# Performance work log

Measured on AMD Instinct MI355X. Metric: run time of the kernel, lower is better.

The kernel has to match this reference:

```python
import jax, jax.numpy as jnp
import numpy as np

V, E, H, TAGS = 50000, 128, 128, 8  # H = hidden per direction (hidden_dim // 2)
B, T = 64, 512


def _lstm_dir(x, w_ih, w_hh, b_ih, b_hh, reverse):
    # x: [B,T,I] -> hs: [B,T,H]; PyTorch gate order i,f,g,o
    xg = jnp.einsum('bti,gi->btg', x, w_ih) + b_ih + b_hh  # [B,T,4H]
    if reverse:
        xg = xg[:, ::-1]
    Bn = x.shape[0]
    Hn = w_hh.shape[1]

    def step(carry, g):
        h, c = carry
        g = g + h @ w_hh.T
        i, f, gg, o = jnp.split(g, 4, axis=-1)
        c = jax.nn.sigmoid(f) * c + jax.nn.sigmoid(i) * jnp.tanh(gg)
        h = jax.nn.sigmoid(o) * jnp.tanh(c)
        return (h, c), h

    h0 = jnp.zeros((Bn, Hn), x.dtype)
    _, hs = jax.lax.scan(step, (h0, h0), jnp.swapaxes(xg, 0, 1))
    hs = jnp.swapaxes(hs, 0, 1)
    return hs[:, ::-1] if reverse else hs


def _crf_partition(emissions, transitions):
    # emissions: [B,T,K]; scan the forward algorithm over time
    fv0 = emissions[:, 0]  # [B,K]

    def step(fv, emit):
        fv = jax.nn.logsumexp(fv[:, :, None] + transitions[None] + emit[:, None, :], axis=1)
        return fv, None

    fv, _ = jax.lax.scan(step, fv0, jnp.swapaxes(emissions[:, 1:], 0, 1))
    return jax.nn.logsumexp(fv, axis=1)  # [B]


def _forward_nll(sentences, tags, embedding, lstm_params, h2t_w, h2t_b, transitions):
    x = embedding[sentences]  # [B,T,E]; dropout inactive (eval)
    for pf, pb in lstm_params:
        x = jnp.concatenate([_lstm_dir(x, *pf, False), _lstm_dir(x, *pb, True)], axis=-1)
    emissions = x @ h2t_w.T + h2t_b  # [B,T,K]
    # gold path score (mask = all ones)
    emit_score = jnp.take_along_axis(emissions, tags[:, :, None], axis=2)[..., 0].sum(axis=1)
    trans_score = transitions[tags[:, :-1], tags[:, 1:]].sum(axis=1)
    partition = _crf_partition(emissions, transitions)
    return -(emit_score + trans_score - partition).mean()


def setup_inputs() -> dict:
    key = jax.random.key(0)
    ks = jax.random.split(key, 40)
    sc = 0.05
    inp = {}
    inp['sentences'] = jax.random.randint(ks[0], (B, T), 0, V)
    inp['tags'] = jax.random.randint(ks[1], (B, T), 0, TAGS)
    emb = jax.random.normal(ks[2], (V, E), jnp.float32) * sc
    inp['embedding'] = emb.at[0].set(0.0)  # padding_idx=0
    idx = 3
    for l in range(2):
        in_dim = E if l == 0 else 2 * H
        for d in ('', '_rev'):
            inp[f'w_ih_l{l}{d}'] = jax.random.normal(ks[idx], (4 * H, in_dim), jnp.float32) * sc; idx += 1
            inp[f'w_hh_l{l}{d}'] = jax.random.normal(ks[idx], (4 * H, H), jnp.float32) * sc; idx += 1
            inp[f'b_ih_l{l}{d}'] = jax.random.normal(ks[idx], (4 * H,), jnp.float32) * sc; idx += 1
            inp[f'b_hh_l{l}{d}'] = jax.random.normal(ks[idx], (4 * H,), jnp.float32) * sc; idx += 1
    inp['h2t_w'] = jax.random.normal(ks[idx], (TAGS, 2 * H), jnp.float32) * sc; idx += 1
    inp['h2t_b'] = jax.random.normal(ks[idx], (TAGS,), jnp.float32) * sc; idx += 1
    trans = jax.random.normal(ks[idx], (TAGS, TAGS), jnp.float32)
    inp['transitions'] = trans.at[0, :].set(-10000.0).at[:, 0].set(-10000.0)
    return inp


def reference(sentences, tags, embedding,
              w_ih_l0, w_hh_l0, b_ih_l0, b_hh_l0,
              w_ih_l0_rev, w_hh_l0_rev, b_ih_l0_rev, b_hh_l0_rev,
              w_ih_l1, w_hh_l1, b_ih_l1, b_hh_l1,
              w_ih_l1_rev, w_hh_l1_rev, b_ih_l1_rev, b_hh_l1_rev,
              h2t_w, h2t_b, transitions):
    lstm_params = [
        ((w_ih_l0, w_hh_l0, b_ih_l0, b_hh_l0), (w_ih_l0_rev, w_hh_l0_rev, b_ih_l0_rev, b_hh_l0_rev)),
        ((w_ih_l1, w_hh_l1, b_ih_l1, b_hh_l1), (w_ih_l1_rev, w_hh_l1_rev, b_ih_l1_rev, b_hh_l1_rev)),
    ]
    return _forward_nll(sentences, tags, embedding, lstm_params, h2t_w, h2t_b, transitions)
```

## Files before the change

kernel.cpp:

```cpp
#include <hip/hip_runtime.h>
#include <cstdint>
#include <cstddef>

typedef __attribute__((ext_vector_type(8))) short bf16x8;
typedef __attribute__((ext_vector_type(8))) int   v8i;
typedef __attribute__((ext_vector_type(4))) float f32x4;

__device__ __forceinline__ unsigned short f2bf(float x) {
    union { float f; unsigned u; } v; v.f = x;
    unsigned r = (v.u + 0x7fffu + ((v.u >> 16) & 1u)) >> 16;
    return (unsigned short)r;
}
__device__ __forceinline__ unsigned short f2bf_trunc(float x) {
    union { float f; unsigned u; } v; v.f = x;
    return (unsigned short)(v.u >> 16);
}
__device__ __forceinline__ float bflo(unsigned u){ union{unsigned i;float f;}v; v.i = u << 16;        return v.f; }
__device__ __forceinline__ float bfhi(unsigned u){ union{unsigned i;float f;}v; v.i = u & 0xffff0000u; return v.f; }
__device__ __forceinline__ float frcp(float x){ return __builtin_amdgcn_rcpf(x); }
__device__ __forceinline__ float fsig(float x){ return frcp(1.f + __expf(-x)); }
__device__ __forceinline__ float ftanh(float x){ return 2.f * frcp(1.f + __expf(-2.f * x)) - 1.f; }

#define BARRIER_LGKM() asm volatile("s_waitcnt lgkmcnt(0)\n\ts_barrier" ::: "memory")

#define BB 64
#define TT 512
#define MM (BB*TT)
#define NG 1024

__device__ __forceinline__ int perm_orig(int g2) {
    return (g2 & 3) * 128 + (g2 >> 6) * 16 + ((g2 >> 4) & 3) * 4 + ((g2 >> 2) & 3);
}

__global__ void prep_kernel(
    const int* __restrict__ sentences, const float* __restrict__ emb,
    const float* __restrict__ w_ih_l0, const float* __restrict__ w_ih_l0r,
    const float* __restrict__ w_ih_l1, const float* __restrict__ w_ih_l1r,
    const float* __restrict__ w_hh_l0, const float* __restrict__ w_hh_l0r,
    const float* __restrict__ w_hh_l1, const float* __restrict__ w_hh_l1r,
    const float* __restrict__ b_ih_l0, const float* __restrict__ b_hh_l0,
    const float* __restrict__ b_ih_l0r, const float* __restrict__ b_hh_l0r,
    const float* __restrict__ b_ih_l1, const float* __restrict__ b_hh_l1,
    const float* __restrict__ b_ih_l1r, const float* __restrict__ b_hh_l1r,
    unsigned short* __restrict__ x0, unsigned short* __restrict__ W0c,
    unsigned short* __restrict__ W1c,
    int* __restrict__ Whh0q, int* __restrict__ Whh1q,
    float* __restrict__ bias0, float* __restrict__ bias1)
{
    int blk = blockIdx.x;
    if (blk < 4096) {
        int t4 = blk * 256 + threadIdx.x;
        int e4 = t4 * 4; int m = e4 >> 7; int k = e4 & 127;
        int tt = m >> 6, b = m & 63;
        int s = sentences[b * 512 + tt];
        float4 v = *(const float4*)(emb + (size_t)s * 128 + k);
        *(ushort4*)(x0 + (size_t)m * 128 + k) =
            make_ushort4(f2bf(v.x), f2bf(v.y), f2bf(v.z), f2bf(v.w));
    } else if (blk < 4224) {
        int t4 = (blk - 4096) * 256 + threadIdx.x;
        int e4 = t4 * 4; int n = e4 >> 7; int k = e4 & 127;
        int dir = n >> 9; int orig = perm_orig(n & 511);
        const float* src = dir ? w_ih_l0r : w_ih_l0;
        float4 v = *(const float4*)(src + (size_t)orig * 128 + k);
        *(ushort4*)(W0c + (size_t)n * 128 + k) =
            make_ushort4(f2bf(v.x), f2bf(v.y), f2bf(v.z), f2bf(v.w));
    } else if (blk < 4480) {
        int t4 = (blk - 4224) * 256 + threadIdx.x;
        int e4 = t4 * 4; int n = e4 >> 8; int k = e4 & 255;
        int dir = n >> 9; int orig = perm_orig(n & 511);
        const float* src = dir ? w_ih_l1r : w_ih_l1;
        float4 v = *(const float4*)(src + (size_t)orig * 256 + k);
        *(ushort4*)(W1c + (size_t)n * 256 + k) =
            make_ushort4(f2bf(v.x), f2bf(v.y), f2bf(v.z), f2bf(v.w));
    } else if (blk < 4736) {
        int lb = blk - 4480;
        int layer = lb >> 7;
        int t4 = (lb & 127) * 256 + threadIdx.x;
        int f  = t4 * 4;
        int j0   = f & 31;
        int lp   = (f >> 5) & 63;
        int quad = lp >> 4, r = lp & 15;
        int tb   = f >> 11;
        int tile = tb & 3, w = (tb >> 2) & 7, dir = tb >> 5;
        int g2 = w * 64 + tile * 16 + r;
        int orig = perm_orig(g2);
        const float* src = layer ? (dir ? w_hh_l1r : w_hh_l1)
                                 : (dir ? w_hh_l0r : w_hh_l0);
        int k = quad * 32 + j0;
        float4 v = *(const float4*)(src + (size_t)orig * 128 + k);
        int p = __builtin_amdgcn_cvt_pk_fp8_f32(v.x * 64.f, v.y * 64.f, 0, false);
        p = __builtin_amdgcn_cvt_pk_fp8_f32(v.z * 64.f, v.w * 64.f, p, true);
        (layer ? Whh1q : Whh0q)[f >> 2] = p;
    } else {
        int t = (blk - 4736) * 256 + threadIdx.x;
        int n = t & 1023;
        int dir = n >> 9; int orig = perm_orig(n & 511);
        if (t < 1024)
            bias0[n] = dir ? (b_ih_l0r[orig] + b_hh_l0r[orig]) : (b_ih_l0[orig] + b_hh_l0[orig]);
        else
            bias1[n] = dir ? (b_ih_l1r[orig] + b_hh_l1r[orig]) : (b_ih_l1[orig] + b_hh_l1[orig]);
    }
}

__global__ __launch_bounds__(256, 2) void gemm_xg(
    const unsigned short* __restrict__ W,
    const unsigned short* __restrict__ X,
    const float* __restrict__ bias,
    unsigned short* __restrict__ xgS,
    int K)
{
    __shared__ unsigned short sW[128 * 32];
    __shared__ unsigned short sX[128 * 32];
    const int tid  = threadIdx.x;
    const int lane = tid & 63;
    const int wid  = tid >> 6;
    const int w_n  = wid & 1, w_m = wid >> 1;
    const int r16  = lane & 15, quad = lane >> 4;
    const int nTile = blockIdx.x * 128;
    const int mTile = blockIdx.y * 128;

    f32x4 zero = {0.f, 0.f, 0.f, 0.f};
    f32x4 acc[4][4];
    #pragma unroll
    for (int i = 0; i < 4; ++i)
        #pragma unroll
        for (int j = 0; j < 4; ++j) acc[i][j] = zero;

    const int q0 = tid, q1 = tid + 256;
    const int r0 = q0 >> 2, c0 = q0 & 3, ko0 = c0 * 8;
    const int r1 = q1 >> 2, c1 = q1 & 3, ko1 = c1 * 8;
    const int s0 = (r0 << 2) | (c0 ^ ((r0 >> 1) & 3));
    const int s1 = (r1 << 2) | (c1 ^ ((r1 >> 1) & 3));
    const int rsw = quad ^ ((r16 >> 1) & 3);

    const unsigned short* Wp0 = W + (size_t)(nTile + r0) * K + ko0;
    const unsigned short* Wp1 = W + (size_t)(nTile + r1) * K + ko1;
    const unsigned short* Xp0 = X + (size_t)(mTile + r0) * K + ko0;
    const unsigned short* Xp1 = X + (size_t)(mTile + r1) * K + ko1;

    uint4 wv0 = *(const uint4*)(Wp0);
    uint4 wv1 = *(const uint4*)(Wp1);
    uint4 xv0 = *(const uint4*)(Xp0);
    uint4 xv1 = *(const uint4*)(Xp1);

    for (int k0 = 0; k0 < K; k0 += 32) {
        BARRIER_LGKM();
        ((uint4*)sW)[s0] = wv0;
        ((uint4*)sW)[s1] = wv1;
        ((uint4*)sX)[s0] = xv0;
        ((uint4*)sX)[s1] = xv1;
        BARRIER_LGKM();
        if (k0 + 32 < K) {
            wv0 = *(const uint4*)(Wp0 + k0 + 32);
            wv1 = *(const uint4*)(Wp1 + k0 + 32);
            xv0 = *(const uint4*)(Xp0 + k0 + 32);
            xv1 = *(const uint4*)(Xp1 + k0 + 32);
        }
        const bf16x8* sWv = (const bf16x8*)sW;
        const bf16x8* sXv = (const bf16x8*)sX;
        bf16x8 a[4], bx[4];
        #pragma unroll
        for (int i = 0; i < 4; ++i) {
            a[i]  = sWv[((w_n * 64 + i * 16 + r16) << 2) | rsw];
            bx[i] = sXv[((w_m * 64 + i * 16 + r16) << 2) | rsw];
        }
        #pragma unroll
        for (int i = 0; i < 4; ++i)
            #pragma unroll
            for (int j = 0; j < 4; ++j)
                acc[i][j] = __builtin_amdgcn_mfma_f32_16x16x32_bf16(a[i], bx[j], acc[i][j], 0, 0, 0);
    }

    const int w_idx = ((nTile & 511) >> 6) + w_n;
    const int dirn  = nTile >> 9;
    float4 bv[4];
    #pragma unroll
    for (int i = 0; i < 4; ++i)
        bv[i] = *(const float4*)(bias + nTile + w_n * 64 + i * 16 + quad * 4);
    const int t  = (mTile >> 6) + w_m;
    const size_t pbase = (size_t)(t >> 1) * 131072 + (size_t)dirn * 65536
                       + (size_t)w_idx * 512 + (size_t)(t & 1) * 4;
    #pragma unroll
    for (int j = 0; j < 4; ++j) {
        int b = j * 16 + r16;
        size_t base = pbase + (size_t)(b >> 2) * 4096;
        #pragma unroll
        for (int i = 0; i < 4; ++i) {
            f32x4 v = acc[i][j];
            ushort4 o = make_ushort4(f2bf(v.x + bv[i].x), f2bf(v.y + bv[i].y),
                                     f2bf(v.z + bv[i].z), f2bf(v.w + bv[i].w));
            *(uint2*)(xgS + base + (size_t)(quad * 16 + i * 4 + (b & 3)) * 8) = *(uint2*)&o;
        }
    }
}

__global__ __launch_bounds__(512, 1) void lstm_scan_mfma(
    const unsigned short* __restrict__ xgS,
    const unsigned char* __restrict__ whh_q,
    unsigned short* __restrict__ xnext)
{
    const int dir = blockIdx.x >> 4;
    const int bg  = blockIdx.x & 15;
    const int tid = threadIdx.x;
    const int w   = tid >> 6;
    const int lane= tid & 63;
    const int q   = lane >> 4;
    const int bl  = lane & 15;
    const int d   = bl >> 2;
    const int b4  = bl & 3;
    const int u   = w * 16 + d * 4 + q;
    const int b   = bg * 4 + b4;

    v8i afrag[4];
    {
        const unsigned char* wb = whh_q + (size_t)dir * 65536 + (size_t)w * 8192 + lane * 32;
        #pragma unroll
        for (int tile = 0; tile < 4; ++tile) {
            uint4 a0 = *(const uint4*)(wb + tile * 2048);
            uint4 a1 = *(const uint4*)(wb + tile * 2048 + 16);
            v8i av; av[0]=a0.x; av[1]=a0.y; av[2]=a0.z; av[3]=a0.w;
                    av[4]=a1.x; av[5]=a1.y; av[6]=a1.z; av[7]=a1.w;
            afrag[tile] = av;
        }
    }

    __shared__ __align__(16) unsigned char hbuf[2][576];
    if (tid < 144) ((unsigned*)hbuf[1])[tid] = 0;

    const f32x4 zero4 = {0.f, 0.f, 0.f, 0.f};

    float c = 0.f;
    const int pstep = dir ? -131072 : 131072;
    const unsigned short* xp = xgS + (size_t)(dir ? 255 : 0) * 131072
                             + (size_t)dir * 65536 + bg * 4096 + w * 512 + lane * 8;
    const int hstep = dir ? -16384 : 16384;
    unsigned short* hp = xnext + (size_t)(dir ? 511 : 0) * 16384 + b * 256 + dir * 128 + u;

    const int hw  = b4 * 144 + u;
    const int hr  = b4 * 144 + q * 32;

    auto step_body = [&](uint2 xv, const unsigned char* rb, unsigned char* wbuf) {
        uint4 h0 = *(const uint4*)(rb + hr);
        uint4 h1 = *(const uint4*)(rb + hr + 16);
        v8i bfr; bfr[0]=h0.x; bfr[1]=h0.y; bfr[2]=h0.z; bfr[3]=h0.w;
                 bfr[4]=h1.x; bfr[5]=h1.y; bfr[6]=h1.z; bfr[7]=h1.w;
        f32x4 a0 = __builtin_amdgcn_mfma_scale_f32_16x16x128_f8f6f4(afrag[0], bfr, zero4, 0, 0,
                       0, 0x79797979, 0, 0x7B7B7B7B);
        f32x4 a1 = __builtin_amdgcn_mfma_scale_f32_16x16x128_f8f6f4(afrag[1], bfr, zero4, 0, 0,
                       0, 0x79797979, 0, 0x7B7B7B7B);
        f32x4 a2 = __builtin_amdgcn_mfma_scale_f32_16x16x128_f8f6f4(afrag[2], bfr, zero4, 0, 0,
                       0, 0x79797979, 0, 0x7B7B7B7B);
        f32x4 a3 = __builtin_amdgcn_mfma_scale_f32_16x16x128_f8f6f4(afrag[3], bfr, zero4, 0, 0,
                       0, 0x79797979, 0, 0x7B7B7B7B);
        f32x4 sel = a0;
        sel = (d == 1) ? a1 : sel;
        sel = (d == 2) ? a2 : sel;
        sel = (d == 3) ? a3 : sel;
        float iv = sel.x + bflo(xv.x);
        float fv = sel.y + bfhi(xv.x);
        float gg = sel.z + bflo(xv.y);
        float ov = sel.w + bfhi(xv.y);
        float si = fsig(iv);
        float sf = fsig(fv);
        float tg = ftanh(gg);
        float so = fsig(ov);
        c = sf * c + si * tg;
        float h = so * ftanh(c);
        *hp = f2bf_trunc(h);
        hp += hstep;
        int q8 = __builtin_amdgcn_cvt_pk_fp8_f32(h * 16.f, h * 16.f, 0, false);
        wbuf[hw] = (unsigned char)(q8 & 0xff);
        BARRIER_LGKM();
    };

    uint4 ring[4];
    #pragma unroll
    for (int i = 0; i < 4; ++i)
        ring[i] = *(const uint4*)(xp + i * pstep);

    BARRIER_LGKM();

    for (int it2 = 0; it2 < 64; ++it2) {
        #pragma unroll
        for (int pp = 0; pp < 4; ++pp) {
            uint4 rv = ring[pp];
            uint2 xa, xb;
            if (dir) { xa.x = rv.z; xa.y = rv.w; xb.x = rv.x; xb.y = rv.y; }
            else     { xa.x = rv.x; xa.y = rv.y; xb.x = rv.z; xb.y = rv.w; }
            ring[pp] = *(const uint4*)(xp + 4 * pstep);
            xp += pstep;
            step_body(xa, hbuf[1], hbuf[0]);
            step_body(xb, hbuf[0], hbuf[1]);
        }
    }
}

__global__ void emis_kernel(const unsigned short* __restrict__ x2,
                            const float* __restrict__ h2t_w,
                            const float* __restrict__ h2t_b,
                            float* __restrict__ emis)
{
    int idx = blockIdx.x * 256 + threadIdx.x;
    int m = idx >> 3, tag = idx & 7;
    const unsigned short* xr = x2 + (size_t)m * 256;
    const float* wr = h2t_w + (size_t)tag * 256;
    float a0 = 0.f, a1 = 0.f, a2 = 0.f, a3 = 0.f;
    #pragma unroll 4
    for (int k = 0; k < 256; k += 8) {
        uint4 xv = *(const uint4*)(xr + k);
        float4 w0 = *(const float4*)(wr + k);
        float4 w1 = *(const float4*)(wr + k + 4);
        a0 += bflo(xv.x) * w0.x + bfhi(xv.x) * w0.y;
        a1 += bflo(xv.y) * w0.z + bfhi(xv.y) * w0.w;
        a2 += bflo(xv.z) * w1.x + bfhi(xv.z) * w1.y;
        a3 += bflo(xv.w) * w1.z + bfhi(xv.w) * w1.w;
    }
    emis[idx] = h2t_b[tag] + ((a0 + a1) + (a2 + a3));
}

__global__ void crf_chunk(const float* __restrict__ emis,
                          const float* __restrict__ trans,
                          float* __restrict__ Pc)
{
    const int b = blockIdx.x >> 3;
    const int cch = blockIdx.x & 7;
    const int l = threadIdx.x;
    const int i = l >> 3, j = l & 7;
    const int i8 = i * 8;
    float T[8];
    #pragma unroll
    for (int k = 0; k < 8; ++k) T[k] = trans[k * 8 + j];

    const int t0 = (cch == 0) ? 1 : cch * 64;
    const int t1 = cch * 64 + 64;
    const float* ej = emis + (size_t)b * 8 + j;

    float P = trans[i * 8 + j] + ej[(size_t)t0 * 512];
    float e1 = ej[(size_t)(t0 + 1) * 512];
    for (int t = t0 + 1; t < t1; ++t) {
        float v0 = __shfl(P, i8 + 0) + T[0];
        float v1 = __shfl(P, i8 + 1) + T[1];
        float v2 = __shfl(P, i8 + 2) + T[2];
        float v3 = __shfl(P, i8 + 3) + T[3];
        float v4 = __shfl(P, i8 + 4) + T[4];
        float v5 = __shfl(P, i8 + 5) + T[5];
        float v6 = __shfl(P, i8 + 6) + T[6];
        float v7 = __shfl(P, i8 + 7) + T[7];
        float m = fmaxf(fmaxf(fmaxf(v0, v1), fmaxf(v2, v3)),
                        fmaxf(fmaxf(v4, v5), fmaxf(v6, v7)));
        float s = __expf(v0 - m) + __expf(v1 - m) + __expf(v2 - m) + __expf(v3 - m)
                + __expf(v4 - m) + __expf(v5 - m) + __expf(v6 - m) + __expf(v7 - m);
        P = m + __logf(s) + e1;
        e1 = ej[(size_t)(t + 1) * 512];
    }
    Pc[((size_t)b * 8 + cch) * 64 + l] = P;
}

__global__ void crf_combine(const float* __restrict__ emis,
                            const float* __restrict__ Pc,
                            const int* __restrict__ tags,
                            const float* __restrict__ trans,
                            float* __restrict__ partials)
{
    const int l = threadIdx.x;
    const int sl = l >> 3, j = l & 7, sl8 = sl * 8;
    const int b = blockIdx.x * 8 + sl;

    float fv = emis[(size_t)b * 8 + j];
    #pragma unroll
    for (int cch = 0; cch < 8; ++cch) {
        const float* Pb = Pc + ((size_t)b * 8 + cch) * 64 + j;
        float p0 = Pb[0],  p1 = Pb[8],  p2 = Pb[16], p3 = Pb[24];
        float p4 = Pb[32], p5 = Pb[40], p6 = Pb[48], p7 = Pb[56];
        float v0 = __shfl(fv, sl8 + 0) + p0;
        float v1 = __shfl(fv, sl8 + 1) + p1;
        float v2 = __shfl(fv, sl8 + 2) + p2;
        float v3 = __shfl(fv, sl8 + 3) + p3;
        float v4 = __shfl(fv, sl8 + 4) + p4;
        float v5 = __shfl(fv, sl8 + 5) + p5;
        float v6 = __shfl(fv, sl8 + 6) + p6;
        float v7 = __shfl(fv, sl8 + 7) + p7;
        float m = fmaxf(fmaxf(fmaxf(v0, v1), fmaxf(v2, v3)),
                        fmaxf(fmaxf(v4, v5), fmaxf(v6, v7)));
        float s = __expf(v0 - m) + __expf(v1 - m) + __expf(v2 - m) + __expf(v3 - m)
                + __expf(v4 - m) + __expf(v5 - m) + __expf(v6 - m) + __expf(v7 - m);
        fv = m + __logf(s);
    }

    float m2 = fv;
    m2 = fmaxf(m2, __shfl_xor(m2, 1));
    m2 = fmaxf(m2, __shfl_xor(m2, 2));
    m2 = fmaxf(m2, __shfl_xor(m2, 4));
    float e2s = __expf(fv - m2);
    e2s += __shfl_xor(e2s, 1);
    e2s += __shfl_xor(e2s, 2);
    e2s += __shfl_xor(e2s, 4);
    float partition = m2 + __logf(e2s);

    const int* tg = tags + (size_t)b * TT;
    float sc = 0.f;
    for (int tt = j; tt < TT; tt += 8) {
        int tag = tg[tt];
        sc += emis[((size_t)tt * 64 + b) * 8 + tag];
        if (tt > 0) sc += trans[tg[tt - 1] * 8 + tag];
    }
    sc += __shfl_xor(sc, 1);
    sc += __shfl_xor(sc, 2);
    sc += __shfl_xor(sc, 4);
    if (j == 0) partials[b] = sc - partition;
}

__global__ void final_kernel(const float* __restrict__ partials, float* __restrict__ out)
{
    int l = threadIdx.x;
    float v = partials[l];
    #pragma unroll
    for (int d = 1; d < 64; d <<= 1) v += __shfl_xor(v, d);
    if (l == 0) out[0] = -v / 64.f;
}

extern "C" void kernel_launch(void* const* d_in, const int* in_sizes, int n_in,
                              void* d_out, int out_size, void* d_ws, size_t ws_size,
                              hipStream_t stream)
{
    const int*   sentences = (const int*)d_in[0];
    const int*   tags      = (const int*)d_in[1];
    const float* embedding = (const float*)d_in[2];
    const float* w_ih_l0   = (const float*)d_in[3];
    const float* w_hh_l0   = (const float*)d_in[4];
    const float* b_ih_l0   = (const float*)d_in[5];
    const float* b_hh_l0   = (const float*)d_in[6];
    const float* w_ih_l0r  = (const float*)d_in[7];
    const float* w_hh_l0r  = (const float*)d_in[8];
    const float* b_ih_l0r  = (const float*)d_in[9];
    const float* b_hh_l0r  = (const float*)d_in[10];
    const float* w_ih_l1   = (const float*)d_in[11];
    const float* w_hh_l1   = (const float*)d_in[12];
    const float* b_ih_l1   = (const float*)d_in[13];
    const float* b_hh_l1   = (const float*)d_in[14];
    const float* w_ih_l1r  = (const float*)d_in[15];
    const float* w_hh_l1r  = (const float*)d_in[16];
    const float* b_ih_l1r  = (const float*)d_in[17];
    const float* b_hh_l1r  = (const float*)d_in[18];
    const float* h2t_w     = (const float*)d_in[19];
    const float* h2t_b     = (const float*)d_in[20];
    const float* trans     = (const float*)d_in[21];

    char* ws = (char*)d_ws;
    unsigned short* W0c   = (unsigned short*)(ws + 0);
    unsigned short* W1c   = (unsigned short*)(ws + 262144);
    int*  Whh0q           = (int*)(ws + 786432);
    int*  Whh1q           = (int*)(ws + 917504);
    float* bias0          = (float*)(ws + 1310720);
    float* bias1          = (float*)(ws + 1314816);
    float* emis           = (float*)(ws + 1318912);
    float* partials       = (float*)(ws + 2375680);
    float* Pc             = (float*)(ws + 2375936);
    unsigned short* xgS   = (unsigned short*)(ws + 4194304);
    unsigned short* x0    = (unsigned short*)(ws + 71303168);
    unsigned short* x1    = (unsigned short*)(ws + 72351744);
    unsigned short* x2    = x1;
    (void)ws_size; (void)in_sizes; (void)n_in; (void)out_size;

    prep_kernel<<<4744, 256, 0, stream>>>(sentences, embedding,
        w_ih_l0, w_ih_l0r, w_ih_l1, w_ih_l1r,
        w_hh_l0, w_hh_l0r, w_hh_l1, w_hh_l1r,
        b_ih_l0, b_hh_l0, b_ih_l0r, b_hh_l0r,
        b_ih_l1, b_hh_l1, b_ih_l1r, b_hh_l1r,
        x0, W0c, W1c, Whh0q, Whh1q, bias0, bias1);

    gemm_xg<<<dim3(8, 256), 256, 0, stream>>>(W0c, x0, bias0, xgS, 128);
    lstm_scan_mfma<<<32, 512, 0, stream>>>(xgS, (const unsigned char*)Whh0q, x1);
    gemm_xg<<<dim3(8, 256), 256, 0, stream>>>(W1c, x1, bias1, xgS, 256);
    lstm_scan_mfma<<<32, 512, 0, stream>>>(xgS, (const unsigned char*)Whh1q, x2);
    emis_kernel<<<1024, 256, 0, stream>>>(x2, h2t_w, h2t_b, emis);
    crf_chunk<<<512, 64, 0, stream>>>(emis, trans, Pc);
    crf_combine<<<8, 64, 0, stream>>>(emis, Pc, tags, trans, partials);
    final_kernel<<<1, 64, 0, stream>>>(partials, (float*)d_out);
}
```

Measured before the change: 645.5 us.

## Prescale gates by -log2e, seed MFMA accumulators with xg, fuse final reduction

Folds the -log2(e) (or -2log2(e) for the tanh gate) factors into both the fp8-quantized recurrent weights and the bf16 input-gate projections. The scan can then apply exp2 directly to the MFMA output, and the input-gate term is passed as the MFMA accumulator instead of being added afterwards. This removes multiplies and adds from the serial per-step critical path. It also removes final_kernel by reducing inside crf_combine with an atomicAdd into a memset output, which adds a memset and makes the summation order nondeterministic.

Measured after the change: 608.9 us. -5.7%, faster.

```diff
diff --git a/kernel.cpp b/kernel.cpp
--- a/kernel.cpp
+++ b/kernel.cpp
@@ -18,8 +18,7 @@
 __device__ __forceinline__ float bflo(unsigned u){ union{unsigned i;float f;}v; v.i = u << 16;        return v.f; }
 __device__ __forceinline__ float bfhi(unsigned u){ union{unsigned i;float f;}v; v.i = u & 0xffff0000u; return v.f; }
 __device__ __forceinline__ float frcp(float x){ return __builtin_amdgcn_rcpf(x); }
-__device__ __forceinline__ float fsig(float x){ return frcp(1.f + __expf(-x)); }
-__device__ __forceinline__ float ftanh(float x){ return 2.f * frcp(1.f + __expf(-2.f * x)) - 1.f; }
+__device__ __forceinline__ float ex2(float x){ return __builtin_amdgcn_exp2f(x); }
 
 #define BARRIER_LGKM() asm volatile("s_waitcnt lgkmcnt(0)\n\ts_barrier" ::: "memory")
 
@@ -27,6 +26,9 @@
 #define TT 512
 #define MM (BB*TT)
 #define NG 1024
+
+#define NL2E  -1.442695f
+#define N2L2E -2.885390f
 
 __device__ __forceinline__ int perm_orig(int g2) {
     return (g2 & 3) * 128 + (g2 >> 6) * 16 + ((g2 >> 4) & 3) * 4 + ((g2 >> 2) & 3);
@@ -87,9 +89,10 @@
         const float* src = layer ? (dir ? w_hh_l1r : w_hh_l1)
                                  : (dir ? w_hh_l0r : w_hh_l0);
         int k = quad * 32 + j0;
+        float fac = ((r & 3) == 2) ? (N2L2E * 64.f) : (NL2E * 64.f);
         float4 v = *(const float4*)(src + (size_t)orig * 128 + k);
-        int p = __builtin_amdgcn_cvt_pk_fp8_f32(v.x * 64.f, v.y * 64.f, 0, false);
-        p = __builtin_amdgcn_cvt_pk_fp8_f32(v.z * 64.f, v.w * 64.f, p, true);
+        int p = __builtin_amdgcn_cvt_pk_fp8_f32(v.x * fac, v.y * fac, 0, false);
+        p = __builtin_amdgcn_cvt_pk_fp8_f32(v.z * fac, v.w * fac, p, true);
         (layer ? Whh1q : Whh0q)[f >> 2] = p;
     } else {
         int t = (blk - 4736) * 256 + threadIdx.x;
@@ -187,8 +190,10 @@
         #pragma unroll
         for (int i = 0; i < 4; ++i) {
             f32x4 v = acc[i][j];
-            ushort4 o = make_ushort4(f2bf(v.x + bv[i].x), f2bf(v.y + bv[i].y),
-                                     f2bf(v.z + bv[i].z), f2bf(v.w + bv[i].w));
+            ushort4 o = make_ushort4(f2bf((v.x + bv[i].x) * NL2E),
+                                     f2bf((v.y + bv[i].y) * NL2E),
+                                     f2bf((v.z + bv[i].z) * N2L2E),
+                                     f2bf((v.w + bv[i].w) * NL2E));
             *(uint2*)(xgS + base + (size_t)(quad * 16 + i * 4 + (b & 3)) * 8) = *(uint2*)&o;
         }
     }
@@ -227,14 +232,12 @@
     __shared__ __align__(16) unsigned char hbuf[2][576];
     if (tid < 144) ((unsigned*)hbuf[1])[tid] = 0;
 
-    const f32x4 zero4 = {0.f, 0.f, 0.f, 0.f};
-
     float c = 0.f;
-    const int pstep = dir ? -131072 : 131072;
+    const long pstep = dir ? -131072L : 131072L;
     const unsigned short* xp = xgS + (size_t)(dir ? 255 : 0) * 131072
                              + (size_t)dir * 65536 + bg * 4096 + w * 512 + lane * 8;
-    const int hstep = dir ? -16384 : 16384;
-    unsigned short* hp = xnext + (size_t)(dir ? 511 : 0) * 16384 + b * 256 + dir * 128 + u;
+    const long hstep = dir ? -16384L : 16384L;
+    long hoff = (long)(dir ? 511 : 0) * 16384 + (long)b * 256 + dir * 128 + u;
 
     const int hw  = b4 * 144 + u;
     const int hr  = b4 * 144 + q * 32;
@@ -244,30 +247,31 @@
         uint4 h1 = *(const uint4*)(rb + hr + 16);
         v8i bfr; bfr[0]=h0.x; bfr[1]=h0.y; bfr[2]=h0.z; bfr[3]=h0.w;
                  bfr[4]=h1.x; bfr[5]=h1.y; bfr[6]=h1.z; bfr[7]=h1.w;
-        f32x4 a0 = __builtin_amdgcn_mfma_scale_f32_16x16x128_f8f6f4(afrag[0], bfr, zero4, 0, 0,
-                       0, 0x79797979, 0, 0x7B7B7B7B);
-        f32x4 a1 = __builtin_amdgcn_mfma_scale_f32_16x16x128_f8f6f4(afrag[1], bfr, zero4, 0, 0,
-                       0, 0x79797979, 0, 0x7B7B7B7B);
-        f32x4 a2 = __builtin_amdgcn_mfma_scale_f32_16x16x128_f8f6f4(afrag[2], bfr, zero4, 0, 0,
-                       0, 0x79797979, 0, 0x7B7B7B7B);
-        f32x4 a3 = __builtin_amdgcn_mfma_scale_f32_16x16x128_f8f6f4(afrag[3], bfr, zero4, 0, 0,
-                       0, 0x79797979, 0, 0x7B7B7B7B);
+        f32x4 gv;
+        gv.x = bflo(xv.x); gv.y = bfhi(xv.x);
+        gv.z = bflo(xv.y); gv.w = bfhi(xv.y);
+        f32x4 a0 = gv, a1 = gv, a2 = gv, a3 = gv;
+        a0 = __builtin_amdgcn_mfma_scale_f32_16x16x128_f8f6f4(afrag[0], bfr, a0, 0, 0,
+                 0, 0x79797979, 0, 0x7B7B7B7B);
+        a1 = __builtin_amdgcn_mfma_scale_f32_16x16x128_f8f6f4(afrag[1], bfr, a1, 0, 0,
+                 0, 0x79797979, 0, 0x7B7B7B7B);
+        a2 = __builtin_amdgcn_mfma_scale_f32_16x16x128_f8f6f4(afrag[2], bfr, a2, 0, 0,
+                 0, 0x79797979, 0, 0x7B7B7B7B);
+        a3 = __builtin_amdgcn_mfma_scale_f32_16x16x128_f8f6f4(afrag[3], bfr, a3, 0, 0,
+                 0, 0x79797979, 0, 0x7B7B7B7B);
         f32x4 sel = a0;
         sel = (d == 1) ? a1 : sel;
         sel = (d == 2) ? a2 : sel;
         sel = (d == 3) ? a3 : sel;
-        float iv = sel.x + bflo(xv.x);
-        float fv = sel.y + bfhi(xv.x);
-        float gg = sel.z + bflo(xv.y);
-        float ov = sel.w + bfhi(xv.y);
-        float si = fsig(iv);
-        float sf = fsig(fv);
-        float tg = ftanh(gg);
-        float so = fsig(ov);
+        float si = frcp(1.f + ex2(sel.x));
+        float sf = frcp(1.f + ex2(sel.y));
+        float tg = 2.f * frcp(1.f + ex2(sel.z)) - 1.f;
+        float so = frcp(1.f + ex2(sel.w));
         c = sf * c + si * tg;
-        float h = so * ftanh(c);
-        *hp = f2bf_trunc(h);
-        hp += hstep;
+        float tc = 2.f * frcp(1.f + ex2(N2L2E * c)) - 1.f;
+        float h = so * tc;
+        xnext[hoff] = f2bf_trunc(h);
+        hoff += hstep;
         int q8 = __builtin_amdgcn_cvt_pk_fp8_f32(h * 16.f, h * 16.f, 0, false);
         wbuf[hw] = (unsigned char)(q8 & 0xff);
         BARRIER_LGKM();
@@ -276,7 +280,7 @@
     uint4 ring[4];
     #pragma unroll
     for (int i = 0; i < 4; ++i)
-        ring[i] = *(const uint4*)(xp + i * pstep);
+        ring[i] = *(const uint4*)(xp + (long)i * pstep);
 
     BARRIER_LGKM();
 
@@ -360,7 +364,7 @@
                             const float* __restrict__ Pc,
                             const int* __restrict__ tags,
                             const float* __restrict__ trans,
-                            float* __restrict__ partials)
+                            float* __restrict__ out)
 {
     const int l = threadIdx.x;
     const int sl = l >> 3, j = l & 7, sl8 = sl * 8;
@@ -407,16 +411,11 @@
     sc += __shfl_xor(sc, 1);
     sc += __shfl_xor(sc, 2);
     sc += __shfl_xor(sc, 4);
-    if (j == 0) partials[b] = sc - partition;
-}
-
-__global__ void final_kernel(const float* __restrict__ partials, float* __restrict__ out)
-{
-    int l = threadIdx.x;
-    float v = partials[l];
-    #pragma unroll
-    for (int d = 1; d < 64; d <<= 1) v += __shfl_xor(v, d);
-    if (l == 0) out[0] = -v / 64.f;
+
+    float val = (j == 0) ? (partition - sc) * 0.015625f : 0.f;
+    #pragma unroll
+    for (int dd = 1; dd < 64; dd <<= 1) val += __shfl_xor(val, dd);
+    if (l == 0) atomicAdd(out, val);
 }
 
 extern "C" void kernel_launch(void* const* d_in, const int* in_sizes, int n_in,
@@ -454,7 +453,6 @@
     float* bias0          = (float*)(ws + 1310720);
     float* bias1          = (float*)(ws + 1314816);
     float* emis           = (float*)(ws + 1318912);
-    float* partials       = (float*)(ws + 2375680);
     float* Pc             = (float*)(ws + 2375936);
     unsigned short* xgS   = (unsigned short*)(ws + 4194304);
     unsigned short* x0    = (unsigned short*)(ws + 71303168);
@@ -462,6 +460,8 @@
     unsigned short* x2    = x1;
     (void)ws_size; (void)in_sizes; (void)n_in; (void)out_size;
 
+    hipMemsetAsync(d_out, 0, sizeof(float), stream);
+
     prep_kernel<<<4744, 256, 0, stream>>>(sentences, embedding,
         w_ih_l0, w_ih_l0r, w_ih_l1, w_ih_l1r,
         w_hh_l0, w_hh_l0r, w_hh_l1, w_hh_l1r,
@@ -475,6 +475,5 @@
     lstm_scan_mfma<<<32, 512, 0, stream>>>(xgS, (const unsigned char*)Whh1q, x2);
     emis_kernel<<<1024, 256, 0, stream>>>(x2, h2t_w, h2t_b, emis);
     crf_chunk<<<512, 64, 0, stream>>>(emis, trans, Pc);
-    crf_combine<<<8, 64, 0, stream>>>(emis, Pc, tags, trans, partials);
-    final_kernel<<<1, 64, 0, stream>>>(partials, (float*)d_out);
-}
+    crf_combine<<<8, 64, 0, stream>>>(emis, Pc, tags, trans, (float*)d_out);
+}
```
